# Kernel tuning notes

Hardware: AMD Instinct MI355X
Metric: run time of the kernel (lower is better)

Reference implementation:

```python
import jax, jax.numpy as jnp
from jax import lax
import numpy as np

EMBED, HIDDEN, VOCAB = 512, 512, 10000
ATT, ENC = 512, 2048
B, NPIX, T = 128, 49, 30


def _lin(k, out_d, in_d):
    k1, k2 = jax.random.split(k)
    s = 1.0 / np.sqrt(in_d)
    return (jax.random.uniform(k1, (out_d, in_d), minval=-s, maxval=s),
            jax.random.uniform(k2, (out_d,), minval=-s, maxval=s))


def setup_inputs() -> dict:
    key = jax.random.key(0)
    ks = jax.random.split(key, 24)
    inp = {}
    inp['enc_image'] = jax.random.normal(ks[0], (B, NPIX, ENC))
    inp['global_features'] = jax.random.normal(ks[1], (B, ENC))
    inp['encoded_captions'] = jax.random.randint(ks[2], (B, T), 0, VOCAB)
    lens = jax.random.randint(ks[3], (B,), 1, T + 1).at[0].set(T)
    inp['caption_lengths'] = lens[:, None]
    # parameters
    inp['emb_W'] = jax.random.uniform(ks[4], (VOCAB, EMBED), minval=-0.1, maxval=0.1)
    inp['e2h_W'], inp['e2h_b'] = _lin(ks[5], HIDDEN, ENC)
    inp['gf_W'], inp['gf_b'] = _lin(ks[6], EMBED, ENC)
    inp['fc_W'] = jax.random.uniform(ks[7], (VOCAB, HIDDEN), minval=-0.1, maxval=0.1)
    inp['fc_b'] = jnp.zeros((VOCAB,))
    inp['lstm_Wih'], inp['lstm_bih'] = _lin(ks[8], 4 * HIDDEN, 2 * EMBED)
    inp['lstm_Whh'], inp['lstm_bhh'] = _lin(ks[9], 4 * HIDDEN, HIDDEN)
    inp['xg_W'], inp['xg_b'] = _lin(ks[10], HIDDEN, 2 * EMBED)
    inp['hg_W'], inp['hg_b'] = _lin(ks[11], HIDDEN, HIDDEN)
    inp['senaff_W'], inp['senaff_b'] = _lin(ks[12], HIDDEN, HIDDEN)
    inp['senatt_W'], inp['senatt_b'] = _lin(ks[13], ATT, HIDDEN)
    inp['haff_W'], inp['haff_b'] = _lin(ks[14], HIDDEN, HIDDEN)
    inp['hatt_W'], inp['hatt_b'] = _lin(ks[15], ATT, HIDDEN)
    inp['vatt_W'], inp['vatt_b'] = _lin(ks[16], ATT, HIDDEN)
    inp['alph_W'], inp['alph_b'] = _lin(ks[17], 1, ATT)
    inp['ctx_W'], inp['ctx_b'] = _lin(ks[18], HIDDEN, HIDDEN)
    return inp


def reference(enc_image, global_features, encoded_captions, caption_lengths,
              emb_W, e2h_W, e2h_b, gf_W, gf_b, fc_W, fc_b,
              lstm_Wih, lstm_bih, lstm_Whh, lstm_bhh,
              xg_W, xg_b, hg_W, hg_b,
              senaff_W, senaff_b, senatt_W, senatt_b,
              haff_W, haff_b, hatt_W, hatt_b,
              vatt_W, vatt_b, alph_W, alph_b, ctx_W, ctx_b):
    lengths = caption_lengths[:, 0]
    order = jnp.argsort(-lengths)                     # descending (stable)
    lengths = lengths[order]
    spatial = jax.nn.relu(jnp.einsum('bpe,he->bph', enc_image[order], e2h_W) + e2h_b)  # (B,NP,H)
    gimg = jax.nn.relu(global_features[order] @ gf_W.T + gf_b)                          # (B,E)
    embs = emb_W[encoded_captions[order]]                                               # (B,T,E)
    inputs = jnp.concatenate([embs, jnp.broadcast_to(gimg[:, None, :], embs.shape)], axis=-1)  # (B,T,2E)
    vattn = jnp.einsum('bph,ah->bpa', spatial, vatt_W) + vatt_b                         # (B,NP,A) hoisted
    h0 = jnp.zeros((spatial.shape[0], HIDDEN), spatial.dtype)
    c0 = h0

    def step(carry, xs):
        h, c = carry
        xt, mask = xs                                  # (B,2E), (B,) bool = row still active
        gates = xt @ lstm_Wih.T + lstm_bih + h @ lstm_Whh.T + lstm_bhh
        i, f, g, o = jnp.split(gates, 4, axis=-1)
        c_new = jax.nn.sigmoid(f) * c + jax.nn.sigmoid(i) * jnp.tanh(g)
        h_new = jax.nn.sigmoid(o) * jnp.tanh(c_new)
        st = jax.nn.sigmoid(xt @ xg_W.T + xg_b + h @ hg_W.T + hg_b) * jnp.tanh(c_new)  # sentinel
        sen_aff = jax.nn.relu(st @ senaff_W.T + senaff_b)    # (B,H)
        sen_att = sen_aff @ senatt_W.T + senatt_b            # (B,A)
        h_aff = jnp.tanh(h_new @ haff_W.T + haff_b)
        h_att = h_aff @ hatt_W.T + hatt_b
        att_feats = jnp.concatenate([vattn, sen_att[:, None, :]], axis=1)   # (B,NP+1,A)
        scores = jnp.tanh(att_feats + h_att[:, None, :]) @ alph_W[0] + alph_b[0]
        alpha = jax.nn.softmax(scores, axis=1)               # (B,NP+1)
        cat_feats = jnp.concatenate([spatial, sen_aff[:, None, :]], axis=1)
        context = jnp.einsum('bph,bp->bh', cat_feats, alpha)
        out_l = jnp.tanh((context + h_aff) @ ctx_W.T + ctx_b)
        pt = out_l @ fc_W.T + fc_b                           # dropout = identity (eval)
        m = mask[:, None]
        return (jnp.where(m, h_new, h), jnp.where(m, c_new, c)), jnp.where(m, pt, 0.0)

    masks = lengths[None, :] > jnp.arange(T)[:, None]        # (T,B) replicates shrinking batch_size_t
    _, preds = lax.scan(step, (h0, c0), (jnp.swapaxes(inputs, 0, 1), masks))
    return jnp.swapaxes(preds, 0, 1)                         # (B,T,VOCAB), sorted-by-length order
```

## Files before the change

### kernel.cpp

```cpp
#include <hip/hip_runtime.h>
#include <hip/hip_bf16.h>
#include <cstdint>
#include <cstddef>

#define DEVI __device__ __forceinline__

#define BB 128
#define TT 30
#define VOCAB 10000
#define ENCD 2048
#define NPIX 49
#define SLOT 65536

typedef __attribute__((ext_vector_type(8))) short bf16x8;
typedef __attribute__((ext_vector_type(4))) float f32x4;

DEVI float bf2f(unsigned short u){ union{float f; unsigned int i;} x; x.i=((unsigned)u)<<16; return x.f; }
DEVI unsigned short f2bf(float f){ union{float f; unsigned int i;} x; x.f=f; unsigned r=x.i + 0x7fffu + ((x.i>>16)&1u); return (unsigned short)(r>>16); }
DEVI float sigm(float x){ return 1.0f/(1.0f+expf(-x)); }
DEVI f32x4 mfma16(bf16x8 a, bf16x8 b, f32x4 c){ return __builtin_amdgcn_mfma_f32_16x16x32_bf16(a,b,c,0,0,0); }

DEVI uint4 byp16(const void* p){
  const unsigned long long* q=(const unsigned long long*)p;
  unsigned long long a=__hip_atomic_load(q,   __ATOMIC_RELAXED, __HIP_MEMORY_SCOPE_AGENT);
  unsigned long long b=__hip_atomic_load(q+1, __ATOMIC_RELAXED, __HIP_MEMORY_SCOPE_AGENT);
  uint4 r; r.x=(unsigned)a; r.y=(unsigned)(a>>32); r.z=(unsigned)b; r.w=(unsigned)(b>>32); return r;
}
DEVI unsigned byp4(const void* p){
  return __hip_atomic_load((const unsigned*)p, __ATOMIC_RELAXED, __HIP_MEMORY_SCOPE_AGENT);
}

DEVI void waitflags(int* flags, int thresh){
  __syncthreads();
  if(threadIdx.x < 64){
    for(;;){
      int v = (threadIdx.x<32) ? __hip_atomic_load(&flags[threadIdx.x], __ATOMIC_RELAXED, __HIP_MEMORY_SCOPE_AGENT)
                               : 0x7fffffff;
      if(__all(v >= thresh)) break;
      __builtin_amdgcn_s_sleep(8);
    }
  }
  asm volatile("" ::: "memory");
  __syncthreads();
}
DEVI void signal(int* flag, int val){
  __syncthreads();
  if(threadIdx.x==0) __hip_atomic_store(flag, val, __ATOMIC_RELEASE, __HIP_MEMORY_SCOPE_AGENT);
}
DEVI void waitdone(int* f, int thresh){
  __syncthreads();
  if(threadIdx.x==0){
    int spins=0;
    while(__hip_atomic_load(f, __ATOMIC_RELAXED, __HIP_MEMORY_SCOPE_AGENT) < thresh){
      if(spins<8) __builtin_amdgcn_s_sleep(4);
      else        __builtin_amdgcn_s_sleep(64);
      spins++;
    }
  }
  asm volatile("" ::: "memory");
  __syncthreads();
}

__global__ void k_sort(const int* __restrict__ lens, int* __restrict__ order, int* __restrict__ Bt){
  __shared__ int L[BB];
  int i = threadIdx.x;
  L[i] = lens[i];
  __syncthreads();
  int li = L[i]; int rank = 0;
  for(int j=0;j<BB;j++){ int lj=L[j]; rank += (lj>li) || (lj==li && j<i); }
  order[rank] = i;
  if(i<TT){ int c=0; for(int j=0;j<BB;j++) c += (L[j]>i); Bt[i]=c; }
}

struct WC13 { const float* src[13]; unsigned short* dst[13]; int n[13]; };
__global__ void k_wconv(WC13 wc){
  int stride = gridDim.x*blockDim.x;
  int tid0 = blockIdx.x*blockDim.x + threadIdx.x;
  for(int s=0;s<13;s++){
    const float4* src=(const float4*)wc.src[s];
    int n4 = wc.n[s]>>2;
    ushort4* dst=(ushort4*)wc.dst[s];
    for(int i=tid0;i<n4;i+=stride){
      float4 v=src[i];
      ushort4 o; o.x=f2bf(v.x); o.y=f2bf(v.y); o.z=f2bf(v.z); o.w=f2bf(v.w);
      dst[i]=o;
    }
  }
}

__global__ void k_xt(const int* __restrict__ caps, const int* __restrict__ order,
                     const float* __restrict__ embW, const unsigned short* __restrict__ gimg,
                     unsigned short* __restrict__ xt){
  int total=BB*TT*1024;
  for(int idx=blockIdx.x*blockDim.x+threadIdx.x; idx<total; idx+=gridDim.x*blockDim.x){
    int k=idx&1023; int bt=idx>>10; int t=bt%TT; int b=bt/TT;
    unsigned short v;
    if(k<512){ int tok=caps[order[b]*TT+t]; v=f2bf(embW[(size_t)tok*512+k]); }
    else v=gimg[b*512+(k-512)];
    xt[idx]=v;
  }
}

__global__ __launch_bounds__(256) void k_gemm_f32A2(
    const float* __restrict__ A, int lda, int rpb, const int* __restrict__ order,
    const unsigned short* __restrict__ W, const float* __restrict__ bias,
    unsigned short* __restrict__ out, int K)
{
  __shared__ unsigned short As[128][136];
  int tid=threadIdx.x, wave=tid>>6, lane=tid&63, l15=lane&15, l4=lane>>4;
  int mb = blockIdx.y*128;
  f32x4 acc[8][4];
  f32x4 z = {0.f,0.f,0.f,0.f};
  #pragma unroll
  for(int i=0;i<8;i++)
    #pragma unroll
    for(int j=0;j<4;j++) acc[i][j]=z;
  int cch=tid&15, r0=tid>>4;
  int nb = blockIdx.x*256 + wave*64;
  for(int kc=0;kc<K;kc+=128){
    __syncthreads();
    #pragma unroll
    for(int rp=0;rp<8;rp++){
      int r=r0+rp*16;
      int m=mb+r;
      int sb = order[m/rpb]*rpb + m%rpb;
      const float* p = A + (size_t)sb*lda + kc + cch*8;
      float4 v0=*(const float4*)p, v1=*(const float4*)(p+4);
      unsigned short* d=&As[r][cch*8];
      d[0]=f2bf(v0.x); d[1]=f2bf(v0.y); d[2]=f2bf(v0.z); d[3]=f2bf(v0.w);
      d[4]=f2bf(v1.x); d[5]=f2bf(v1.y); d[6]=f2bf(v1.z); d[7]=f2bf(v1.w);
    }
    __syncthreads();
    #pragma unroll
    for(int kk=0;kk<4;kk++){
      bf16x8 bfr[4];
      #pragma unroll
      for(int nt=0;nt<4;nt++)
        bfr[nt] = *(const bf16x8*)(W + (size_t)(nb+nt*16+l15)*K + kc + kk*32 + l4*8);
      #pragma unroll
      for(int mt=0;mt<8;mt++){
        bf16x8 af = *(const bf16x8*)&As[mt*16+l15][kk*32+l4*8];
        #pragma unroll
        for(int nt=0;nt<4;nt++) acc[mt][nt]=mfma16(af,bfr[nt],acc[mt][nt]);
      }
    }
  }
  #pragma unroll
  for(int nt=0;nt<4;nt++){
    int n = nb + nt*16 + l15;
    float bs = bias[n];
    #pragma unroll
    for(int mt=0;mt<8;mt++){
      #pragma unroll
      for(int j=0;j<4;j++){
        int row = mb + mt*16 + l4*4 + j;
        float v = acc[mt][nt][j]+bs; v = v>0.f ? v : 0.f;
        out[(size_t)row*512 + n] = f2bf(v);
      }
    }
  }
}

template<int BYP>
DEVI void dev_gemm512(unsigned short (*As)[136], const unsigned short* A, const unsigned short* W,
                      const float* bias, unsigned short* out, int act, int xtile, int mb){
  int tid=threadIdx.x, wave=tid>>6, lane=tid&63, l15=lane&15, l4=lane>>4;
  f32x4 acc[8];
  f32x4 z = {0.f,0.f,0.f,0.f};
  #pragma unroll
  for(int i=0;i<8;i++) acc[i]=z;
  int cch=tid&15, r0=tid>>4;
  int nrow = xtile*64 + wave*16 + l15;
  for(int kc=0;kc<512;kc+=128){
    __syncthreads();
    #pragma unroll
    for(int rp=0;rp<8;rp++){
      int r=r0+rp*16;
      const unsigned short* src = A + (size_t)(mb+r)*512 + kc + cch*8;
      if(BYP) *(uint4*)&As[r][cch*8] = byp16(src);
      else    *(uint4*)&As[r][cch*8] = *(const uint4*)src;
    }
    __syncthreads();
    #pragma unroll
    for(int kk=0;kk<4;kk++){
      bf16x8 bfr = *(const bf16x8*)(W + (size_t)nrow*512 + kc + kk*32 + l4*8);
      #pragma unroll
      for(int mt=0;mt<8;mt++){
        bf16x8 af = *(const bf16x8*)&As[mt*16+l15][kk*32+l4*8];
        acc[mt]=mfma16(af,bfr,acc[mt]);
      }
    }
  }
  float bs = bias ? bias[nrow] : 0.f;
  #pragma unroll
  for(int mt=0;mt<8;mt++){
    #pragma unroll
    for(int j=0;j<4;j++){
      int row = mb + mt*16 + l4*4 + j;
      float v = acc[mt][j]+bs;
      if(act==1) v = fmaxf(v,0.f);
      else if(act==2) v = tanhf(v);
      out[(size_t)row*512+nrow]=f2bf(v);
    }
  }
  __syncthreads();
}

struct PreD { const unsigned short* A; const unsigned short* W; const float* bias; unsigned short* out; };
struct PreD2 { PreD d[2]; };
__global__ __launch_bounds__(256) void k_pre(PreD2 dd){
  __shared__ unsigned short As[128][136];
  PreD g = dd.d[blockIdx.z];
  dev_gemm512<0>(As, g.A, g.W, g.bias, g.out, 0, blockIdx.x, blockIdx.y*128);
}

struct PCtx {
  const unsigned short *xt, *w_ih, *w_hh, *w_xg, *w_hg;
  const unsigned short *w_saff, *w_satt, *w_haff, *w_hatt, *w_ctx, *w_fc;
  const unsigned short *vattn, *SC;
  const float *bih,*bhh,*bxg,*bhg, *sab,*stbias,*hab,*htb, *alW,*alb, *cxb, *fcb;
  const int *Bt;
  unsigned short *h_hist;
  unsigned short *stb;
  unsigned short *tbuf;
  float *dout;
  int *Lflag;
  int *Ldone;
  int *Tflag;
};

DEVI void dev_lstm(unsigned short (*As)[136], const PCtx& p, int t, int jblk,
                   const unsigned short* hprev, unsigned short* hout, float creg[2][4]){
  int tid=threadIdx.x, wave=tid>>6, lane=tid&63, l15=lane&15, l4=lane>>4;
  int jb = jblk*16;
  f32x4 acc[2][5];
  f32x4 z = {0.f,0.f,0.f,0.f};
  #pragma unroll
  for(int m=0;m<2;m++)
    #pragma unroll
    for(int s=0;s<5;s++) acc[m][s]=z;
  int cch=tid&15, r0=tid>>4;
  for(int kc=0;kc<1536;kc+=128){
    __syncthreads();
    #pragma unroll
    for(int rp=0;rp<8;rp++){
      int r=r0+rp*16;
      int kg = kc + cch*8;
      if(kg<1024){
        *(uint4*)&As[r][cch*8] = *(const uint4*)(p.xt + (size_t)r*(TT*1024) + t*1024 + kg);
      } else {
        *(uint4*)&As[r][cch*8] = byp16(hprev + (size_t)r*512 + (kg-1024));
      }
    }
    __syncthreads();
    #pragma unroll
    for(int kk=0;kk<4;kk++){
      int kg = kc + kk*32 + l4*8;
      bf16x8 bfr[5];
      #pragma unroll
      for(int s=0;s<5;s++){
        int row = (s<4) ? (s*512 + jb + l15) : (jb + l15);
        const unsigned short* wp;
        if(s<4) wp = (kg<1024) ? (p.w_ih + (size_t)row*1024 + kg) : (p.w_hh + (size_t)row*512 + (kg-1024));
        else    wp = (kg<1024) ? (p.w_xg + (size_t)row*1024 + kg) : (p.w_hg + (size_t)row*512 + (kg-1024));
        bfr[s] = *(const bf16x8*)wp;
      }
      #pragma unroll
      for(int m=0;m<2;m++){
        int mt = wave*2+m;
        bf16x8 af = *(const bf16x8*)&As[mt*16+l15][kk*32+l4*8];
        #pragma unroll
        for(int s=0;s<5;s++) acc[m][s]=mfma16(af,bfr[s],acc[m][s]);
      }
    }
  }
  int bt = p.Bt[t];
  int j = jb + l15;
  float bi  = p.bih[j]      + p.bhh[j];
  float bff = p.bih[512+j]  + p.bhh[512+j];
  float bg  = p.bih[1024+j] + p.bhh[1024+j];
  float bo  = p.bih[1536+j] + p.bhh[1536+j];
  float bs  = p.bxg[j] + p.bhg[j];
  unsigned short* stt = p.stb + (size_t)t*SLOT;
  #pragma unroll
  for(int m=0;m<2;m++){
    int mt = wave*2+m;
    #pragma unroll
    for(int jj=0;jj<4;jj++){
      int b = mt*16 + l4*4 + jj;
      float iv = sigm(acc[m][0][jj]+bi);
      float fv = sigm(acc[m][1][jj]+bff);
      float gv = tanhf(acc[m][2][jj]+bg);
      float ov = sigm(acc[m][3][jj]+bo);
      float sv = sigm(acc[m][4][jj]+bs);
      float cn = fv*creg[m][jj] + iv*gv;
      float tc = tanhf(cn);
      size_t idx=(size_t)b*512+j;
      if(b<bt){ hout[idx]=f2bf(ov*tc); creg[m][jj]=cn; }
      else {
        unsigned pr = byp4(hprev + (idx & ~(size_t)1));
        hout[idx] = (j&1) ? (unsigned short)(pr>>16) : (unsigned short)pr;
      }
      stt[idx]=f2bf(sv*tc);
    }
  }
}

DEVI void dev_attn(float* sS, float* sA, unsigned short* sHA, unsigned short* sSA,
                   int b, const PCtx& p,
                   const unsigned short* satt, const unsigned short* hatt,
                   const unsigned short* scs, const unsigned short* sch,
                   unsigned short* outl){
  int tid=threadIdx.x;
  if(tid<64)       *(uint4*)&sHA[tid*8] = byp16(hatt + (size_t)b*512 + tid*8);
  else if(tid<128){ int q=tid-64; *(uint4*)&sSA[q*8] = byp16(satt + (size_t)b*512 + q*8); }
  __syncthreads();
  int gid=tid>>4, gl=tid&15;
  #pragma unroll
  for(int rp=0;rp<4;rp++){
    int pp = rp*16 + gid;
    float s = 0.f;
    if(pp<50){
      if(pp<NPIX){
        const unsigned short* vp = p.vattn + ((size_t)b*NPIX + pp)*512;
        for(int k=gl*32;k<gl*32+32;k++) s += tanhf(bf2f(vp[k]) + bf2f(sHA[k])) * p.alW[k];
      } else {
        for(int k=gl*32;k<gl*32+32;k++) s += tanhf(bf2f(sSA[k]) + bf2f(sHA[k])) * p.alW[k];
      }
    }
    #pragma unroll
    for(int off=8;off>=1;off>>=1) s += __shfl_xor(s, off);
    if(gl==0 && pp<50) sS[pp] = s + p.alb[0];
  }
  __syncthreads();
  if(tid<64){
    float sv = (tid<50) ? sS[tid] : -1e30f;
    float m = sv;
    #pragma unroll
    for(int off=32;off>=1;off>>=1) m = fmaxf(m, __shfl_xor(m, off));
    float e = (tid<50) ? expf(sv-m) : 0.f;
    float sum = e;
    #pragma unroll
    for(int off=32;off>=1;off>>=1) sum += __shfl_xor(sum, off);
    if(tid<50) sA[tid] = e/sum;
  }
  __syncthreads();
  float a49 = sA[49];
  {
    int n0 = tid*2;
    unsigned schU = byp4(sch + (size_t)b*512 + n0);
    unsigned scsU = byp4(scs + (size_t)b*512 + n0);
    float c0 = bf2f((unsigned short)schU), c1 = bf2f((unsigned short)(schU>>16));
    float s0 = bf2f((unsigned short)scsU), s1 = bf2f((unsigned short)(scsU>>16));
    float acc0 = c0 + a49*s0 + p.cxb[n0];
    float acc1 = c1 + a49*s1 + p.cxb[n0+1];
    const unsigned short* sp = p.SC + (size_t)b*NPIX*512 + n0;
    for(int pp=0;pp<NPIX;pp++){
      unsigned u = *(const unsigned*)(sp + (size_t)pp*512);
      acc0 += sA[pp]*bf2f((unsigned short)u);
      acc1 += sA[pp]*bf2f((unsigned short)(u>>16));
    }
    unsigned o = ((unsigned)f2bf(tanhf(acc1))<<16) | (unsigned)f2bf(tanhf(acc0));
    *(unsigned*)(outl + (size_t)b*512 + n0) = o;
  }
  __syncthreads();
}

DEVI void dev_fc_all(unsigned short (*As2)[520], const PCtx& p, int t, int w,
                     const unsigned short* outl){
  int tid=threadIdx.x;
  __syncthreads();
  #pragma unroll
  for(int i=0;i<32;i++){
    int idx = i*256 + tid;
    int r = idx>>6, c = (idx&63)<<3;
    *(uint4*)&As2[r][c] = byp16(outl + (size_t)r*512 + c);
  }
  __syncthreads();
  int wave=tid>>6, lane=tid&63, l15=lane&15, l4=lane>>4;
  int bt = p.Bt[t];
  for(int x=w; x<157; x+=32){
    f32x4 acc[8];
    f32x4 z = {0.f,0.f,0.f,0.f};
    #pragma unroll
    for(int i=0;i<8;i++) acc[i]=z;
    int nbase = x*64 + wave*16;
    int nr = nbase + l15; if(nr > VOCAB-1) nr = VOCAB-1;
    #pragma unroll 4
    for(int kk=0;kk<16;kk++){
      bf16x8 bfr = *(const bf16x8*)(p.w_fc + (size_t)nr*512 + kk*32 + l4*8);
      #pragma unroll
      for(int mt=0;mt<8;mt++){
        if(mt*16 < bt){
          bf16x8 af = *(const bf16x8*)&As2[mt*16+l15][kk*32+l4*8];
          acc[mt]=mfma16(af,bfr,acc[mt]);
        }
      }
    }
    int n = nbase + l15; bool nok = n < VOCAB;
    float bs = nok ? p.fcb[n] : 0.f;
    #pragma unroll
    for(int mt=0;mt<8;mt++){
      #pragma unroll
      for(int j=0;j<4;j++){
        int b = mt*16 + l4*4 + j;
        float v = (b<bt) ? (acc[mt][j]+bs) : 0.f;
        if(nok) p.dout[(size_t)b*(TT*VOCAB) + (size_t)t*VOCAB + n] = v;
      }
    }
  }
  __syncthreads();
}

__global__ __launch_bounds__(256) void k_persist(PCtx p){
  __shared__ __align__(16) char smem[133760];
  auto As  = (unsigned short (*)[136])smem;
  auto As2 = (unsigned short (*)[520])smem;
  float* sS = (float*)(smem + 133120);
  float* sA = sS + 52;
  unsigned short* sHA = (unsigned short*)smem;
  unsigned short* sSA = sHA + 512;
  int cb = blockIdx.x;
  if(cb < 32){
    float creg[2][4];
    #pragma unroll
    for(int m=0;m<2;m++)
      #pragma unroll
      for(int j=0;j<4;j++) creg[m][j]=0.f;
    for(int t=0;t<TT;t++){
      if(t>0){
        waitflags(p.Lflag, t);
        if(cb==0 && threadIdx.x==0)
          __hip_atomic_store(p.Ldone, t, __ATOMIC_RELEASE, __HIP_MEMORY_SCOPE_AGENT);
      }
      dev_lstm(As, p, t, cb, p.h_hist + (size_t)t*SLOT, p.h_hist + (size_t)(t+1)*SLOT, creg);
      signal(&p.Lflag[cb], t+1);
    }
    if(cb==0){
      waitflags(p.Lflag, TT);
      if(threadIdx.x==0)
        __hip_atomic_store(p.Ldone, TT, __ATOMIC_RELEASE, __HIP_MEMORY_SCOPE_AGENT);
    }
  } else {
    int team = (cb-32)>>5, w = (cb-32)&31;
    unsigned short* S = p.tbuf + (size_t)team*7*SLOT;
    unsigned short *Saff=S, *Haff=S+SLOT, *Outl=S+2*SLOT, *Satt=S+3*SLOT,
                   *Hatt=S+4*SLOT, *Scs=S+5*SLOT, *Sch=S+6*SLOT;
    int* tf = p.Tflag + team*32;
    int it=0;
    for(int t=team; t<TT; t+=7, it++){
      waitdone(p.Ldone, t+1);
      if(w<8)       dev_gemm512<1>(As, p.stb + (size_t)t*SLOT,        p.w_saff, p.sab, Saff, 1, w,   0);
      else if(w<16) dev_gemm512<1>(As, p.h_hist + (size_t)(t+1)*SLOT, p.w_haff, p.hab, Haff, 2, w-8, 0);
      signal(&tf[w], it*3+1); waitflags(tf, it*3+1);
      if(w<8)       dev_gemm512<1>(As, Saff, p.w_satt, p.stbias, Satt, 0, w,    0);
      else if(w<16) dev_gemm512<1>(As, Haff, p.w_hatt, p.htb,    Hatt, 0, w-8,  0);
      else if(w<24) dev_gemm512<1>(As, Saff, p.w_ctx,  nullptr,  Scs,  0, w-16, 0);
      else          dev_gemm512<1>(As, Haff, p.w_ctx,  nullptr,  Sch,  0, w-24, 0);
      signal(&tf[w], it*3+2); waitflags(tf, it*3+2);
      for(int r=0;r<4;r++) dev_attn(sS, sA, sHA, sSA, w*4+r, p, Satt, Hatt, Scs, Sch, Outl);
      signal(&tf[w], it*3+3); waitflags(tf, it*3+3);
      dev_fc_all(As2, p, t, w, Outl);
    }
  }
}

extern "C" void kernel_launch(void* const* d_in, const int* in_sizes, int n_in,
                              void* d_out, int out_size, void* d_ws, size_t ws_size,
                              hipStream_t stream)
{
  const float* enc  =(const float*)d_in[0];
  const float* gfeat=(const float*)d_in[1];
  const int*   caps =(const int*)d_in[2];
  const int*   lens =(const int*)d_in[3];
  const float* embW =(const float*)d_in[4];
  const float* e2hW =(const float*)d_in[5];  const float* e2hb=(const float*)d_in[6];
  const float* gfW  =(const float*)d_in[7];  const float* gfb =(const float*)d_in[8];
  const float* fcW  =(const float*)d_in[9];  const float* fcb =(const float*)d_in[10];
  const float* WihF =(const float*)d_in[11]; const float* bih =(const float*)d_in[12];
  const float* WhhF =(const float*)d_in[13]; const float* bhh =(const float*)d_in[14];
  const float* xgWF =(const float*)d_in[15]; const float* bxg =(const float*)d_in[16];
  const float* hgWF =(const float*)d_in[17]; const float* bhg =(const float*)d_in[18];
  const float* saWF =(const float*)d_in[19]; const float* sab =(const float*)d_in[20];
  const float* stWF =(const float*)d_in[21]; const float* stbias=(const float*)d_in[22];
  const float* haWF =(const float*)d_in[23]; const float* hab =(const float*)d_in[24];
  const float* htWF =(const float*)d_in[25]; const float* htb =(const float*)d_in[26];
  const float* vaWF =(const float*)d_in[27]; const float* vab =(const float*)d_in[28];
  const float* alW  =(const float*)d_in[29]; const float* alb =(const float*)d_in[30];
  const float* cxWF =(const float*)d_in[31]; const float* cxb =(const float*)d_in[32];

  char* base=(char*)d_ws; size_t off=0;
  auto alloc=[&](size_t bytes)->void*{ void* r=base+off; off += (bytes+255)&~(size_t)255; return r; };

  int* order=(int*)alloc(BB*4);
  int* Bt   =(int*)alloc(32*4);
  unsigned short* w_e2h =(unsigned short*)alloc((size_t)512*2048*2);
  unsigned short* w_gf  =(unsigned short*)alloc((size_t)512*2048*2);
  unsigned short* w_fc  =(unsigned short*)alloc((size_t)VOCAB*512*2);
  unsigned short* w_ih  =(unsigned short*)alloc((size_t)2048*1024*2);
  unsigned short* w_hh  =(unsigned short*)alloc((size_t)2048*512*2);
  unsigned short* w_xg  =(unsigned short*)alloc((size_t)512*1024*2);
  unsigned short* w_hg  =(unsigned short*)alloc((size_t)512*512*2);
  unsigned short* w_saff=(unsigned short*)alloc((size_t)512*512*2);
  unsigned short* w_satt=(unsigned short*)alloc((size_t)512*512*2);
  unsigned short* w_haff=(unsigned short*)alloc((size_t)512*512*2);
  unsigned short* w_hatt=(unsigned short*)alloc((size_t)512*512*2);
  unsigned short* w_vatt=(unsigned short*)alloc((size_t)512*512*2);
  unsigned short* w_ctx =(unsigned short*)alloc((size_t)512*512*2);
  unsigned short* spatial=(unsigned short*)alloc((size_t)BB*NPIX*512*2);
  unsigned short* vattn  =(unsigned short*)alloc((size_t)BB*NPIX*512*2);
  unsigned short* SC     =(unsigned short*)alloc((size_t)BB*NPIX*512*2);
  unsigned short* gimg   =(unsigned short*)alloc((size_t)BB*512*2);
  unsigned short* xt     =(unsigned short*)alloc((size_t)BB*TT*1024*2);
  int* flags =(int*)alloc(4096);
  unsigned short* tbuf=(unsigned short*)alloc((size_t)7*7*SLOT*2);

  unsigned short* stb_hist = w_e2h;
  unsigned short* h_hist   = spatial;

  k_sort<<<1,BB,0,stream>>>(lens, order, Bt);

  WC13 wc;
  const float* srcs[13] = {e2hW,gfW,fcW,WihF,WhhF,xgWF,hgWF,saWF,stWF,haWF,htWF,vaWF,cxWF};
  unsigned short* dsts[13] = {w_e2h,w_gf,w_fc,w_ih,w_hh,w_xg,w_hg,w_saff,w_satt,w_haff,w_hatt,w_vatt,w_ctx};
  int ns[13] = {512*2048,512*2048,VOCAB*512,2048*1024,2048*512,512*1024,512*512,512*512,512*512,512*512,512*512,512*512,512*512};
  for(int i=0;i<13;i++){ wc.src[i]=srcs[i]; wc.dst[i]=dsts[i]; wc.n[i]=ns[i]; }
  k_wconv<<<1024,256,0,stream>>>(wc);

  k_gemm_f32A2<<<dim3(2,NPIX),256,0,stream>>>(enc, ENCD, NPIX, order, w_e2h, e2hb, spatial, ENCD);
  k_gemm_f32A2<<<dim3(2,1),  256,0,stream>>>(gfeat, ENCD, 1, order, w_gf, gfb, gimg, ENCD);
  k_xt<<<1024,256,0,stream>>>(caps, order, embW, gimg, xt);
  {
    PreD2 dv{};
    dv.d[0] = PreD{spatial, w_vatt, vab,     vattn};
    dv.d[1] = PreD{spatial, w_ctx,  nullptr, SC};
    k_pre<<<dim3(8,NPIX,2),256,0,stream>>>(dv);
  }

  hipMemsetAsync(h_hist, 0, (size_t)SLOT*2, stream);
  hipMemsetAsync(flags, 0, 4096, stream);

  PCtx pc;
  pc.xt=xt; pc.w_ih=w_ih; pc.w_hh=w_hh; pc.w_xg=w_xg; pc.w_hg=w_hg;
  pc.w_saff=w_saff; pc.w_satt=w_satt; pc.w_haff=w_haff; pc.w_hatt=w_hatt; pc.w_ctx=w_ctx; pc.w_fc=w_fc;
  pc.vattn=vattn; pc.SC=SC;
  pc.bih=bih; pc.bhh=bhh; pc.bxg=bxg; pc.bhg=bhg;
  pc.sab=sab; pc.stbias=stbias; pc.hab=hab; pc.htb=htb;
  pc.alW=alW; pc.alb=alb; pc.cxb=cxb; pc.fcb=fcb;
  pc.Bt=Bt;
  pc.h_hist=h_hist; pc.stb=stb_hist; pc.tbuf=tbuf;
  pc.dout=(float*)d_out;
  pc.Lflag=flags; pc.Ldone=flags+32; pc.Tflag=flags+64;

  k_persist<<<256,256,0,stream>>>(pc);
}
```

Baseline: 2.290 ms.

## Precompute LSTM input projections and pipeline post-LSTM stages across dedicated block groups

The input-side LSTM and sentinel projections (x_t times W_ih and W_xg, plus biases) are hoisted out of the recurrent loop into a separate batched GEMM kernel over all timesteps, which cuts the serial per-step K from 1536 to 512. The persistent kernel's seven time-interleaved teams are replaced by a stage pipeline: dedicated block groups run the affine GEMMs, the attention GEMMs, the attention/context step and the vocab FC, each chained by per-stage flags and per-timestep scratch buffers. This targets the critical-path latency of the recurrence and lets downstream stages overlap across timesteps. The cost is extra memory for the Gx and per-timestep buffers, more flag traffic, and bf16 rounding of the precomputed gate inputs.

Result: slower. 3.061 ms (+33.7%).

```diff
diff --git a/kernel.cpp b/kernel.cpp
--- a/kernel.cpp
+++ b/kernel.cpp
@@ -30,12 +30,12 @@
   return __hip_atomic_load((const unsigned*)p, __ATOMIC_RELAXED, __HIP_MEMORY_SCOPE_AGENT);
 }
 
-DEVI void waitflags(int* flags, int thresh){
+DEVI void waitflags(int* flags, int n, int thresh){
   __syncthreads();
   if(threadIdx.x < 64){
     for(;;){
-      int v = (threadIdx.x<32) ? __hip_atomic_load(&flags[threadIdx.x], __ATOMIC_RELAXED, __HIP_MEMORY_SCOPE_AGENT)
-                               : 0x7fffffff;
+      int v = (threadIdx.x<n) ? __hip_atomic_load(&flags[threadIdx.x], __ATOMIC_RELAXED, __HIP_MEMORY_SCOPE_AGENT)
+                              : 0x7fffffff;
       if(__all(v >= thresh)) break;
       __builtin_amdgcn_s_sleep(8);
     }
@@ -46,6 +46,10 @@
 DEVI void signal(int* flag, int val){
   __syncthreads();
   if(threadIdx.x==0) __hip_atomic_store(flag, val, __ATOMIC_RELEASE, __HIP_MEMORY_SCOPE_AGENT);
+}
+DEVI void publish(int* flag, int val){
+  if(threadIdx.x==0) __hip_atomic_store(flag, val, __ATOMIC_RELEASE, __HIP_MEMORY_SCOPE_AGENT);
+  __syncthreads();
 }
 DEVI void waitdone(int* f, int thresh){
   __syncthreads();
@@ -53,7 +57,7 @@
     int spins=0;
     while(__hip_atomic_load(f, __ATOMIC_RELAXED, __HIP_MEMORY_SCOPE_AGENT) < thresh){
       if(spins<8) __builtin_amdgcn_s_sleep(4);
-      else        __builtin_amdgcn_s_sleep(64);
+      else        __builtin_amdgcn_s_sleep(32);
       spins++;
     }
   }
@@ -163,7 +167,7 @@
 
 template<int BYP>
 DEVI void dev_gemm512(unsigned short (*As)[136], const unsigned short* A, const unsigned short* W,
-                      const float* bias, unsigned short* out, int act, int xtile, int mb){
+                      const float* bias, unsigned short* out, int act, int xtile){
   int tid=threadIdx.x, wave=tid>>6, lane=tid&63, l15=lane&15, l4=lane>>4;
   f32x4 acc[8];
   f32x4 z = {0.f,0.f,0.f,0.f};
@@ -176,7 +180,7 @@
     #pragma unroll
     for(int rp=0;rp<8;rp++){
       int r=r0+rp*16;
-      const unsigned short* src = A + (size_t)(mb+r)*512 + kc + cch*8;
+      const unsigned short* src = A + (size_t)r*512 + kc + cch*8;
       if(BYP) *(uint4*)&As[r][cch*8] = byp16(src);
       else    *(uint4*)&As[r][cch*8] = *(const uint4*)src;
     }
@@ -196,7 +200,7 @@
   for(int mt=0;mt<8;mt++){
     #pragma unroll
     for(int j=0;j<4;j++){
-      int row = mb + mt*16 + l4*4 + j;
+      int row = mt*16 + l4*4 + j;
       float v = acc[mt][j]+bs;
       if(act==1) v = fmaxf(v,0.f);
       else if(act==2) v = tanhf(v);
@@ -211,46 +215,91 @@
 __global__ __launch_bounds__(256) void k_pre(PreD2 dd){
   __shared__ unsigned short As[128][136];
   PreD g = dd.d[blockIdx.z];
-  dev_gemm512<0>(As, g.A, g.W, g.bias, g.out, 0, blockIdx.x, blockIdx.y*128);
+  dev_gemm512<0>(As, g.A + (size_t)blockIdx.y*128*512, g.W, g.bias,
+                 g.out + (size_t)blockIdx.y*128*512, 0, blockIdx.x);
+}
+
+__global__ __launch_bounds__(256) void k_gx(
+    const unsigned short* __restrict__ xt, const unsigned short* __restrict__ w_ih,
+    const unsigned short* __restrict__ w_xg,
+    const float* __restrict__ bih, const float* __restrict__ bhh,
+    const float* __restrict__ bxg, const float* __restrict__ bhg,
+    unsigned short* __restrict__ Gx)
+{
+  __shared__ unsigned short As[128][136];
+  int tid=threadIdx.x, wave=tid>>6, lane=tid&63, l15=lane&15, l4=lane>>4;
+  int t = blockIdx.y;
+  f32x4 acc[8];
+  f32x4 z = {0.f,0.f,0.f,0.f};
+  #pragma unroll
+  for(int i=0;i<8;i++) acc[i]=z;
+  int cch=tid&15, r0=tid>>4;
+  int n = blockIdx.x*64 + wave*16 + l15;
+  const unsigned short* wrow = (n<2048) ? (w_ih + (size_t)n*1024) : (w_xg + (size_t)(n-2048)*1024);
+  for(int kc=0;kc<1024;kc+=128){
+    __syncthreads();
+    #pragma unroll
+    for(int rp=0;rp<8;rp++){
+      int r=r0+rp*16;
+      *(uint4*)&As[r][cch*8] = *(const uint4*)(xt + (size_t)r*(TT*1024) + t*1024 + kc + cch*8);
+    }
+    __syncthreads();
+    #pragma unroll
+    for(int kk=0;kk<4;kk++){
+      bf16x8 bfr = *(const bf16x8*)(wrow + kc + kk*32 + l4*8);
+      #pragma unroll
+      for(int mt=0;mt<8;mt++){
+        bf16x8 af = *(const bf16x8*)&As[mt*16+l15][kk*32+l4*8];
+        acc[mt]=mfma16(af,bfr,acc[mt]);
+      }
+    }
+  }
+  float bias = (n<2048) ? (bih[n]+bhh[n]) : (bxg[n-2048]+bhg[n-2048]);
+  #pragma unroll
+  for(int mt=0;mt<8;mt++){
+    int row = mt*16 + l4*4;
+    ushort4 o;
+    o.x=f2bf(acc[mt][0]+bias); o.y=f2bf(acc[mt][1]+bias);
+    o.z=f2bf(acc[mt][2]+bias); o.w=f2bf(acc[mt][3]+bias);
+    *(ushort4*)(Gx + ((size_t)t*2560 + n)*128 + row) = o;
+  }
 }
 
 struct PCtx {
-  const unsigned short *xt, *w_ih, *w_hh, *w_xg, *w_hg;
+  const unsigned short *w_hh, *w_hg, *Gx;
   const unsigned short *w_saff, *w_satt, *w_haff, *w_hatt, *w_ctx, *w_fc;
   const unsigned short *vattn, *SC;
-  const float *bih,*bhh,*bxg,*bhg, *sab,*stbias,*hab,*htb, *alW,*alb, *cxb, *fcb;
+  const float *sab,*stbias,*hab,*htb, *alW,*alb, *cxb, *fcb;
   const int *Bt;
   unsigned short *h_hist;
   unsigned short *stb;
-  unsigned short *tbuf;
+  unsigned short *sbuf;
   float *dout;
-  int *Lflag;
-  int *Ldone;
-  int *Tflag;
+  int *Lflag,*Ldone,*SAfA,*Adone,*SBf,*Bdone,*S3f,*S3done;
 };
 
-DEVI void dev_lstm(unsigned short (*As)[136], const PCtx& p, int t, int jblk,
-                   const unsigned short* hprev, unsigned short* hout, float creg[2][4]){
+DEVI void dev_lstm2(unsigned short (*As)[136], const PCtx& p, int t, int jblk,
+                    const unsigned short* hprev, unsigned short* hout, float creg[2][4]){
   int tid=threadIdx.x, wave=tid>>6, lane=tid&63, l15=lane&15, l4=lane>>4;
   int jb = jblk*16;
   f32x4 acc[2][5];
-  f32x4 z = {0.f,0.f,0.f,0.f};
-  #pragma unroll
-  for(int m=0;m<2;m++)
-    #pragma unroll
-    for(int s=0;s<5;s++) acc[m][s]=z;
+  #pragma unroll
+  for(int m=0;m<2;m++){
+    #pragma unroll
+    for(int s=0;s<5;s++){
+      int col = (s<4) ? (s*512 + jb + l15) : (2048 + jb + l15);
+      int row = (wave*2+m)*16 + l4*4;
+      ushort4 g = *(const ushort4*)(p.Gx + ((size_t)t*2560 + col)*128 + row);
+      acc[m][s][0]=bf2f(g.x); acc[m][s][1]=bf2f(g.y); acc[m][s][2]=bf2f(g.z); acc[m][s][3]=bf2f(g.w);
+    }
+  }
   int cch=tid&15, r0=tid>>4;
-  for(int kc=0;kc<1536;kc+=128){
+  for(int kc=0;kc<512;kc+=128){
     __syncthreads();
     #pragma unroll
     for(int rp=0;rp<8;rp++){
       int r=r0+rp*16;
-      int kg = kc + cch*8;
-      if(kg<1024){
-        *(uint4*)&As[r][cch*8] = *(const uint4*)(p.xt + (size_t)r*(TT*1024) + t*1024 + kg);
-      } else {
-        *(uint4*)&As[r][cch*8] = byp16(hprev + (size_t)r*512 + (kg-1024));
-      }
+      *(uint4*)&As[r][cch*8] = byp16(hprev + (size_t)r*512 + kc + cch*8);
     }
     __syncthreads();
     #pragma unroll
@@ -259,16 +308,13 @@
       bf16x8 bfr[5];
       #pragma unroll
       for(int s=0;s<5;s++){
-        int row = (s<4) ? (s*512 + jb + l15) : (jb + l15);
-        const unsigned short* wp;
-        if(s<4) wp = (kg<1024) ? (p.w_ih + (size_t)row*1024 + kg) : (p.w_hh + (size_t)row*512 + (kg-1024));
-        else    wp = (kg<1024) ? (p.w_xg + (size_t)row*1024 + kg) : (p.w_hg + (size_t)row*512 + (kg-1024));
+        const unsigned short* wp = (s<4) ? (p.w_hh + (size_t)(s*512+jb+l15)*512 + kg)
+                                         : (p.w_hg + (size_t)(jb+l15)*512 + kg);
         bfr[s] = *(const bf16x8*)wp;
       }
       #pragma unroll
       for(int m=0;m<2;m++){
-        int mt = wave*2+m;
-        bf16x8 af = *(const bf16x8*)&As[mt*16+l15][kk*32+l4*8];
+        bf16x8 af = *(const bf16x8*)&As[(wave*2+m)*16+l15][kk*32+l4*8];
         #pragma unroll
         for(int s=0;s<5;s++) acc[m][s]=mfma16(af,bfr[s],acc[m][s]);
       }
@@ -276,11 +322,6 @@
   }
   int bt = p.Bt[t];
   int j = jb + l15;
-  float bi  = p.bih[j]      + p.bhh[j];
-  float bff = p.bih[512+j]  + p.bhh[512+j];
-  float bg  = p.bih[1024+j] + p.bhh[1024+j];
-  float bo  = p.bih[1536+j] + p.bhh[1536+j];
-  float bs  = p.bxg[j] + p.bhg[j];
   unsigned short* stt = p.stb + (size_t)t*SLOT;
   #pragma unroll
   for(int m=0;m<2;m++){
@@ -288,11 +329,11 @@
     #pragma unroll
     for(int jj=0;jj<4;jj++){
       int b = mt*16 + l4*4 + jj;
-      float iv = sigm(acc[m][0][jj]+bi);
-      float fv = sigm(acc[m][1][jj]+bff);
-      float gv = tanhf(acc[m][2][jj]+bg);
-      float ov = sigm(acc[m][3][jj]+bo);
-      float sv = sigm(acc[m][4][jj]+bs);
+      float iv = sigm(acc[m][0][jj]);
+      float fv = sigm(acc[m][1][jj]);
+      float gv = tanhf(acc[m][2][jj]);
+      float ov = sigm(acc[m][3][jj]);
+      float sv = sigm(acc[m][4][jj]);
       float cn = fv*creg[m][jj] + iv*gv;
       float tc = tanhf(cn);
       size_t idx=(size_t)b*512+j;
@@ -323,8 +364,10 @@
     if(pp<50){
       if(pp<NPIX){
         const unsigned short* vp = p.vattn + ((size_t)b*NPIX + pp)*512;
+        #pragma unroll 8
         for(int k=gl*32;k<gl*32+32;k++) s += tanhf(bf2f(vp[k]) + bf2f(sHA[k])) * p.alW[k];
       } else {
+        #pragma unroll 8
         for(int k=gl*32;k<gl*32+32;k++) s += tanhf(bf2f(sSA[k]) + bf2f(sHA[k])) * p.alW[k];
       }
     }
@@ -355,6 +398,7 @@
     float acc0 = c0 + a49*s0 + p.cxb[n0];
     float acc1 = c1 + a49*s1 + p.cxb[n0+1];
     const unsigned short* sp = p.SC + (size_t)b*NPIX*512 + n0;
+    #pragma unroll 7
     for(int pp=0;pp<NPIX;pp++){
       unsigned u = *(const unsigned*)(sp + (size_t)pp*512);
       acc0 += sA[pp]*bf2f((unsigned short)u);
@@ -366,8 +410,8 @@
   __syncthreads();
 }
 
-DEVI void dev_fc_all(unsigned short (*As2)[520], const PCtx& p, int t, int w,
-                     const unsigned short* outl){
+DEVI void dev_fc2(unsigned short (*As2)[520], const PCtx& p, int t, int f,
+                  const unsigned short* outl){
   int tid=threadIdx.x;
   __syncthreads();
   #pragma unroll
@@ -379,7 +423,7 @@
   __syncthreads();
   int wave=tid>>6, lane=tid&63, l15=lane&15, l4=lane>>4;
   int bt = p.Bt[t];
-  for(int x=w; x<157; x+=32){
+  for(int x=f; x<157; x+=112){
     f32x4 acc[8];
     f32x4 z = {0.f,0.f,0.f,0.f};
     #pragma unroll
@@ -416,11 +460,12 @@
   __shared__ __align__(16) char smem[133760];
   auto As  = (unsigned short (*)[136])smem;
   auto As2 = (unsigned short (*)[520])smem;
-  float* sS = (float*)(smem + 133120);
-  float* sA = sS + 52;
   unsigned short* sHA = (unsigned short*)smem;
   unsigned short* sSA = sHA + 512;
+  float* sS = (float*)(smem + 2048);
+  float* sA = sS + 64;
   int cb = blockIdx.x;
+
   if(cb < 32){
     float creg[2][4];
     #pragma unroll
@@ -429,38 +474,55 @@
       for(int j=0;j<4;j++) creg[m][j]=0.f;
     for(int t=0;t<TT;t++){
       if(t>0){
-        waitflags(p.Lflag, t);
+        waitflags(p.Lflag, 32, t);
         if(cb==0 && threadIdx.x==0)
           __hip_atomic_store(p.Ldone, t, __ATOMIC_RELEASE, __HIP_MEMORY_SCOPE_AGENT);
       }
-      dev_lstm(As, p, t, cb, p.h_hist + (size_t)t*SLOT, p.h_hist + (size_t)(t+1)*SLOT, creg);
+      dev_lstm2(As, p, t, cb, p.h_hist + (size_t)t*SLOT, p.h_hist + (size_t)(t+1)*SLOT, creg);
       signal(&p.Lflag[cb], t+1);
     }
     if(cb==0){
-      waitflags(p.Lflag, TT);
-      if(threadIdx.x==0)
-        __hip_atomic_store(p.Ldone, TT, __ATOMIC_RELEASE, __HIP_MEMORY_SCOPE_AGENT);
+      waitflags(p.Lflag, 32, TT);
+      publish(p.Ldone, TT);
+    }
+  } else if(cb < 48){
+    int w = cb-32;
+    for(int t=0;t<TT;t++){
+      waitdone(p.Ldone, t+1);
+      unsigned short* S = p.sbuf + (size_t)t*7*SLOT;
+      if(w<8) dev_gemm512<1>(As, p.stb + (size_t)t*SLOT,          p.w_saff, p.sab, S,        1, w);
+      else    dev_gemm512<1>(As, p.h_hist + (size_t)(t+1)*SLOT,   p.w_haff, p.hab, S+SLOT,   2, w-8);
+      signal(&p.SAfA[w], t+1);
+      if(w==0){ waitflags(p.SAfA, 16, t+1); publish(p.Adone, t+1); }
+    }
+  } else if(cb < 80){
+    int w = cb-48;
+    for(int t=0;t<TT;t++){
+      waitdone(p.Adone, t+1);
+      unsigned short* S = p.sbuf + (size_t)t*7*SLOT;
+      if(w<8)       dev_gemm512<1>(As, S,      p.w_satt, p.stbias, S+2*SLOT, 0, w);
+      else if(w<16) dev_gemm512<1>(As, S+SLOT, p.w_hatt, p.htb,    S+3*SLOT, 0, w-8);
+      else if(w<24) dev_gemm512<1>(As, S,      p.w_ctx,  nullptr,  S+4*SLOT, 0, w-16);
+      else          dev_gemm512<1>(As, S+SLOT, p.w_ctx,  nullptr,  S+5*SLOT, 0, w-24);
+      signal(&p.SBf[w], t+1);
+      if(w==0){ waitflags(p.SBf, 32, t+1); publish(p.Bdone, t+1); }
+    }
+  } else if(cb < 144){
+    int w = cb-80;
+    for(int t=0;t<TT;t++){
+      waitdone(p.Bdone, t+1);
+      unsigned short* S = p.sbuf + (size_t)t*7*SLOT;
+      dev_attn(sS,sA,sHA,sSA, w*2,   p, S+2*SLOT, S+3*SLOT, S+4*SLOT, S+5*SLOT, S+6*SLOT);
+      dev_attn(sS,sA,sHA,sSA, w*2+1, p, S+2*SLOT, S+3*SLOT, S+4*SLOT, S+5*SLOT, S+6*SLOT);
+      signal(&p.S3f[w], t+1);
+      if(w==0){ waitflags(p.S3f, 64, t+1); publish(p.S3done, t+1); }
     }
   } else {
-    int team = (cb-32)>>5, w = (cb-32)&31;
-    unsigned short* S = p.tbuf + (size_t)team*7*SLOT;
-    unsigned short *Saff=S, *Haff=S+SLOT, *Outl=S+2*SLOT, *Satt=S+3*SLOT,
-                   *Hatt=S+4*SLOT, *Scs=S+5*SLOT, *Sch=S+6*SLOT;
-    int* tf = p.Tflag + team*32;
-    int it=0;
-    for(int t=team; t<TT; t+=7, it++){
-      waitdone(p.Ldone, t+1);
-      if(w<8)       dev_gemm512<1>(As, p.stb + (size_t)t*SLOT,        p.w_saff, p.sab, Saff, 1, w,   0);
-      else if(w<16) dev_gemm512<1>(As, p.h_hist + (size_t)(t+1)*SLOT, p.w_haff, p.hab, Haff, 2, w-8, 0);
-      signal(&tf[w], it*3+1); waitflags(tf, it*3+1);
-      if(w<8)       dev_gemm512<1>(As, Saff, p.w_satt, p.stbias, Satt, 0, w,    0);
-      else if(w<16) dev_gemm512<1>(As, Haff, p.w_hatt, p.htb,    Hatt, 0, w-8,  0);
-      else if(w<24) dev_gemm512<1>(As, Saff, p.w_ctx,  nullptr,  Scs,  0, w-16, 0);
-      else          dev_gemm512<1>(As, Haff, p.w_ctx,  nullptr,  Sch,  0, w-24, 0);
-      signal(&tf[w], it*3+2); waitflags(tf, it*3+2);
-      for(int r=0;r<4;r++) dev_attn(sS, sA, sHA, sSA, w*4+r, p, Satt, Hatt, Scs, Sch, Outl);
-      signal(&tf[w], it*3+3); waitflags(tf, it*3+3);
-      dev_fc_all(As2, p, t, w, Outl);
+    int f = cb-144;
+    for(int t=0;t<TT;t++){
+      waitdone(p.S3done, t+1);
+      unsigned short* S = p.sbuf + (size_t)t*7*SLOT;
+      dev_fc2(As2, p, t, f, S+6*SLOT);
     }
   }
 }
@@ -512,8 +574,9 @@
   unsigned short* SC     =(unsigned short*)alloc((size_t)BB*NPIX*512*2);
   unsigned short* gimg   =(unsigned short*)alloc((size_t)BB*512*2);
   unsigned short* xt     =(unsigned short*)alloc((size_t)BB*TT*1024*2);
-  int* flags =(int*)alloc(4096);
-  unsigned short* tbuf=(unsigned short*)alloc((size_t)7*7*SLOT*2);
+  int* flags =(int*)alloc(8192);
+  unsigned short* Gx  =(unsigned short*)alloc((size_t)TT*2560*128*2);
+  unsigned short* sbuf=(unsigned short*)alloc((size_t)TT*7*SLOT*2);
 
   unsigned short* stb_hist = w_e2h;
   unsigned short* h_hist   = spatial;
@@ -536,21 +599,28 @@
     dv.d[1] = PreD{spatial, w_ctx,  nullptr, SC};
     k_pre<<<dim3(8,NPIX,2),256,0,stream>>>(dv);
   }
+  k_gx<<<dim3(40,TT),256,0,stream>>>(xt, w_ih, w_xg, bih, bhh, bxg, bhg, Gx);
 
   hipMemsetAsync(h_hist, 0, (size_t)SLOT*2, stream);
-  hipMemsetAsync(flags, 0, 4096, stream);
+  hipMemsetAsync(flags, 0, 8192, stream);
 
   PCtx pc;
-  pc.xt=xt; pc.w_ih=w_ih; pc.w_hh=w_hh; pc.w_xg=w_xg; pc.w_hg=w_hg;
+  pc.w_hh=w_hh; pc.w_hg=w_hg; pc.Gx=Gx;
   pc.w_saff=w_saff; pc.w_satt=w_satt; pc.w_haff=w_haff; pc.w_hatt=w_hatt; pc.w_ctx=w_ctx; pc.w_fc=w_fc;
   pc.vattn=vattn; pc.SC=SC;
-  pc.bih=bih; pc.bhh=bhh; pc.bxg=bxg; pc.bhg=bhg;
   pc.sab=sab; pc.stbias=stbias; pc.hab=hab; pc.htb=htb;
   pc.alW=alW; pc.alb=alb; pc.cxb=cxb; pc.fcb=fcb;
   pc.Bt=Bt;
-  pc.h_hist=h_hist; pc.stb=stb_hist; pc.tbuf=tbuf;
+  pc.h_hist=h_hist; pc.stb=stb_hist; pc.sbuf=sbuf;
   pc.dout=(float*)d_out;
-  pc.Lflag=flags; pc.Ldone=flags+32; pc.Tflag=flags+64;
+  pc.Lflag=flags;
+  pc.Ldone=flags+64;
+  pc.SAfA=flags+96;
+  pc.Adone=flags+160;
+  pc.SBf=flags+192;
+  pc.Bdone=flags+256;
+  pc.S3f=flags+288;
+  pc.S3done=flags+416;
 
   k_persist<<<256,256,0,stream>>>(pc);
 }
```
